# Optimization experiments

Hardware: AMD Instinct MI355X
Metric: run time of the kernel (lower is better)

Reference implementation:

```python
import jax, jax.numpy as jnp
import numpy as np

N, IN_C, OUT_C = 8192, 256, 256


def setup_inputs() -> dict:
    key = jax.random.key(0)
    k1, k2, k3 = jax.random.split(key, 3)
    x = jax.random.normal(k1, (N, IN_C), dtype=jnp.float32)
    adj = jax.random.uniform(k2, (N, N), dtype=jnp.float32)
    # learned parameter: torch.rand(in_channels, out_channels)
    w = jax.random.uniform(k3, (IN_C, OUT_C), dtype=jnp.float32)
    return {"x": x, "adj": adj, "w": w}


def reference(x, adj, w):
    # A = adj + I
    A = adj + jnp.eye(adj.shape[0], dtype=adj.dtype)
    # D_hat = sqrt(inv(diag(rowsum(A)))) == diag(deg^{-1/2}) since D is diagonal
    deg = jnp.sum(A, axis=1)                      # [N]
    d_isqrt = jax.lax.rsqrt(deg)                  # [N]
    # A_hat = D_hat @ A @ D_hat  ==  row/col scaling by d^{-1/2}
    A_hat = A * d_isqrt[:, None] * d_isqrt[None, :]
    # ELU((A_hat @ x) @ w)
    h = jnp.matmul(A_hat, x)                      # [N, in_c]
    return jax.nn.elu(jnp.matmul(h, w))           # [N, out_c]
```

## Files before the change

### kernel.cpp

```cpp
#include <hip/hip_runtime.h>
#include <stdint.h>

#define N_NODES 8192
#define CH 256
#define MT 32
#define BK 64
#define KB_COUNT 128
#define NSTAGE 4
#define ZROWS 16
#define ZBLOCKS (N_NODES / ZROWS)
#define DEGBLOCKS (N_NODES / 4)

typedef __bf16 bf16x8 __attribute__((ext_vector_type(8)));
typedef float f32x4 __attribute__((ext_vector_type(4)));
typedef unsigned short u16x4 __attribute__((ext_vector_type(4)));

__device__ __forceinline__ void async_copy16(const void* g, void* l) {
  __builtin_amdgcn_global_load_lds(
      (const __attribute__((address_space(1))) void*)(uintptr_t)g,
      (__attribute__((address_space(3))) void*)(uint32_t)(uintptr_t)l,
      16, 0, 0);
}

__device__ __forceinline__ unsigned short f32_to_bf16_rne(float f) {
  unsigned u = __float_as_uint(f);
  u += 0x7FFFu + ((u >> 16) & 1u);
  return (unsigned short)(u >> 16);
}

__device__ __forceinline__ u16x4 f32x4_to_bf16_rne(f32x4 v) {
  u16x4 r;
  r.x = f32_to_bf16_rne(v.x);
  r.y = f32_to_bf16_rne(v.y);
  r.z = f32_to_bf16_rne(v.z);
  r.w = f32_to_bf16_rne(v.w);
  return r;
}

__global__ void __launch_bounds__(256) k_pass1(const float* __restrict__ x,
                                               const float* __restrict__ w,
                                               const float* __restrict__ adj,
                                               float* __restrict__ z,
                                               float* __restrict__ dsq,
                                               unsigned short* __restrict__ adjb) {
  __shared__ float xs[ZROWS][CH];
  if (blockIdx.x < ZBLOCKS) {
    const int r0 = blockIdx.x * ZROWS;
    const int t = threadIdx.x;
#pragma unroll
    for (int r = 0; r < ZROWS; ++r) xs[r][t] = x[(size_t)(r0 + r) * CH + t];
    __syncthreads();
    float acc[ZROWS];
#pragma unroll
    for (int r = 0; r < ZROWS; ++r) acc[r] = 0.f;
    for (int k = 0; k < CH; k += 8) {
      float wv[8];
#pragma unroll
      for (int u = 0; u < 8; ++u) wv[u] = w[(size_t)(k + u) * CH + t];
#pragma unroll
      for (int r = 0; r < ZROWS; ++r) {
#pragma unroll
        for (int u = 0; u < 8; ++u) acc[r] += xs[r][k + u] * wv[u];
      }
    }
#pragma unroll
    for (int r = 0; r < ZROWS; ++r) z[(size_t)(r0 + r) * CH + t] = acc[r];
  } else {
    const int wave = threadIdx.x >> 6, lane = threadIdx.x & 63;
    const int row = (blockIdx.x - ZBLOCKS) * 4 + wave;
    const f32x4* ar = (const f32x4*)(adj + (size_t)row * N_NODES);
    u16x4* br = (u16x4*)(adjb + (size_t)row * N_NODES);
    float s0 = 0.f, s1 = 0.f, s2 = 0.f, s3 = 0.f;
#pragma unroll
    for (int i = 0; i < 8; ++i) {
      f32x4 a = ar[lane + 64 * (4 * i + 0)];
      f32x4 b = ar[lane + 64 * (4 * i + 1)];
      f32x4 c = ar[lane + 64 * (4 * i + 2)];
      f32x4 d = ar[lane + 64 * (4 * i + 3)];
      br[lane + 64 * (4 * i + 0)] = f32x4_to_bf16_rne(a);
      br[lane + 64 * (4 * i + 1)] = f32x4_to_bf16_rne(b);
      br[lane + 64 * (4 * i + 2)] = f32x4_to_bf16_rne(c);
      br[lane + 64 * (4 * i + 3)] = f32x4_to_bf16_rne(d);
      s0 += (a.x + a.y) + (a.z + a.w);
      s1 += (b.x + b.y) + (b.z + b.w);
      s2 += (c.x + c.y) + (c.z + c.w);
      s3 += (d.x + d.y) + (d.z + d.w);
    }
    float s = (s0 + s1) + (s2 + s3);
#pragma unroll
    for (int off = 32; off > 0; off >>= 1) s += __shfl_down(s, off, 64);
    if (lane == 0) dsq[row] = rsqrtf(s + 1.0f);
  }
}

__global__ void __launch_bounds__(256) k_y(const float* __restrict__ z,
                                           const float* __restrict__ dsq,
                                           unsigned short* __restrict__ yt) {
  const int r0 = blockIdx.x * 16;
  const int t = threadIdx.x;
  unsigned short vals[16];
#pragma unroll
  for (int r = 0; r < 16; ++r)
    vals[r] = f32_to_bf16_rne(dsq[r0 + r] * z[(size_t)(r0 + r) * CH + t]);
  *(u16x4*)&yt[(size_t)t * N_NODES + r0 + 0] = *(u16x4*)&vals[0];
  *(u16x4*)&yt[(size_t)t * N_NODES + r0 + 4] = *(u16x4*)&vals[4];
  *(u16x4*)&yt[(size_t)t * N_NODES + r0 + 8] = *(u16x4*)&vals[8];
  *(u16x4*)&yt[(size_t)t * N_NODES + r0 + 12] = *(u16x4*)&vals[12];
}

__global__ void __launch_bounds__(512, 1) k_gemm1(const unsigned short* __restrict__ adjb,
                                                  const unsigned short* __restrict__ yt,
                                                  const float* __restrict__ z,
                                                  const float* __restrict__ dsq,
                                                  float* __restrict__ out) {
  __shared__ __align__(16) unsigned short As[NSTAGE][MT * BK];
  __shared__ __align__(16) unsigned short Bs[NSTAGE][CH * BK];

  const int tid = threadIdx.x;
  const int wave = tid >> 6;
  const int lane = tid & 63;
  const int m0 = blockIdx.x * MT;
  const int lr = lane & 15;
  const int lq = lane >> 4;

  const bool hasA = wave < 4;
  const unsigned short* ag;
  int aoffu;
  {
    int i = hasA ? wave : 0;
    int p = 64 * i + lane;
    int r = p >> 3;
    int c8 = (lane & 7) ^ (r & 7);
    ag = adjb + (size_t)(m0 + r) * N_NODES + c8 * 8;
    aoffu = 1024 * i;
  }
  const unsigned short* bg[4];
  int boffu[4];
#pragma unroll
  for (int q = 0; q < 4; ++q) {
    int i = wave * 4 + q;
    int p = 64 * i + lane;
    int n = p >> 3;
    int c8 = (lane & 7) ^ (n & 7);
    bg[q] = yt + (size_t)n * N_NODES + c8 * 8;
    boffu[q] = 1024 * i;
  }

  f32x4 acc[2][2];
#pragma unroll
  for (int i = 0; i < 2; ++i)
#pragma unroll
    for (int j = 0; j < 2; ++j) acc[i][j] = (f32x4){0.f, 0.f, 0.f, 0.f};

  auto issue = [&](int b, int k0) {
    char* aL = (char*)&As[b][0];
    char* bL = (char*)&Bs[b][0];
    if (hasA) async_copy16(ag + k0, aL + aoffu);
#pragma unroll
    for (int q = 0; q < 4; ++q) async_copy16(bg[q] + k0, bL + boffu[q]);
  };

  auto compute = [&](int b) {
    const char* aB = (const char*)&As[b][0];
    const char* bB = (const char*)&Bs[b][0];
#pragma unroll
    for (int k32 = 0; k32 < 2; ++k32) {
      bf16x8 afr[2];
#pragma unroll
      for (int mt = 0; mt < 2; ++mt) {
        int row = mt * 16 + lr;
        int c8 = k32 * 4 + lq;
        int p = row * 8 + (c8 ^ (row & 7));
        afr[mt] = *(const bf16x8*)(aB + p * 16);
      }
      __builtin_amdgcn_s_setprio(1);
#pragma unroll
      for (int nt = 0; nt < 2; ++nt) {
        int n = wave * 32 + nt * 16 + lr;
        int c8 = k32 * 4 + lq;
        int p = n * 8 + (c8 ^ (n & 7));
        bf16x8 bfr = *(const bf16x8*)(bB + p * 16);
        acc[0][nt] = __builtin_amdgcn_mfma_f32_16x16x32_bf16(afr[0], bfr, acc[0][nt], 0, 0, 0);
        acc[1][nt] = __builtin_amdgcn_mfma_f32_16x16x32_bf16(afr[1], bfr, acc[1][nt], 0, 0, 0);
      }
      __builtin_amdgcn_s_setprio(0);
    }
  };

  issue(0, 0);
  issue(1, BK);
  issue(2, 2 * BK);

  for (int kb = 0; kb < KB_COUNT - 2; ++kb) {
    if (hasA) asm volatile("s_waitcnt vmcnt(10)" ::: "memory");
    else      asm volatile("s_waitcnt vmcnt(8)"  ::: "memory");
    __builtin_amdgcn_s_barrier();
    __builtin_amdgcn_sched_barrier(0);
    if (kb + 3 < KB_COUNT) issue((kb + 3) & (NSTAGE - 1), (kb + 3) * BK);
    compute(kb & (NSTAGE - 1));
    __builtin_amdgcn_sched_barrier(0);
  }
  if (hasA) asm volatile("s_waitcnt vmcnt(5)" ::: "memory");
  else      asm volatile("s_waitcnt vmcnt(4)" ::: "memory");
  __builtin_amdgcn_s_barrier();
  __builtin_amdgcn_sched_barrier(0);
  compute((KB_COUNT - 2) & (NSTAGE - 1));
  __builtin_amdgcn_sched_barrier(0);
  asm volatile("s_waitcnt vmcnt(0)" ::: "memory");
  __builtin_amdgcn_s_barrier();
  __builtin_amdgcn_sched_barrier(0);
  compute((KB_COUNT - 1) & (NSTAGE - 1));

#pragma unroll
  for (int mt = 0; mt < 2; ++mt) {
#pragma unroll
    for (int r = 0; r < 4; ++r) {
      int row = m0 + mt * 16 + lq * 4 + r;
      float di = dsq[row];
#pragma unroll
      for (int nt = 0; nt < 2; ++nt) {
        int col = wave * 32 + nt * 16 + lr;
        float v = acc[mt][nt][r];
        v = di * (v + di * z[(size_t)row * CH + col]);
        v = v > 0.f ? v : expm1f(v);
        out[(size_t)row * CH + col] = v;
      }
    }
  }
}

extern "C" void kernel_launch(void* const* d_in, const int* in_sizes, int n_in,
                              void* d_out, int out_size, void* d_ws, size_t ws_size,
                              hipStream_t stream) {
  const float* x = (const float*)d_in[0];
  const float* adj = (const float*)d_in[1];
  const float* w = (const float*)d_in[2];
  float* out = (float*)d_out;

  float* dsq = (float*)d_ws;
  unsigned short* yt = (unsigned short*)((char*)d_ws + 32768);
  float* z = (float*)((char*)d_ws + 4227072);
  unsigned short* adjb = (unsigned short*)((char*)d_ws + 12615680);

  k_pass1<<<ZBLOCKS + DEGBLOCKS, 256, 0, stream>>>(x, w, adj, z, dsq, adjb);
  k_y<<<N_NODES / 16, 256, 0, stream>>>(z, dsq, yt);
  k_gemm1<<<N_NODES / MT, 512, 0, stream>>>(adjb, yt, z, dsq, out);
}
```

Before: 480.6 us.

## Use 128-row tiles with 4-way split-K and a separate finalize kernel

```diff
diff --git a/kernel.cpp b/kernel.cpp
--- a/kernel.cpp
+++ b/kernel.cpp
@@ -3,10 +3,12 @@
 
 #define N_NODES 8192
 #define CH 256
-#define MT 32
+#define BM 128
 #define BK 64
-#define KB_COUNT 128
-#define NSTAGE 4
+#define KSPLIT 4
+#define KLEN (N_NODES / KSPLIT)
+#define TILES (KLEN / BK)
+#define NSTAGE 3
 #define ZROWS 16
 #define ZBLOCKS (N_NODES / ZROWS)
 #define DEGBLOCKS (N_NODES / 4)
@@ -110,54 +112,57 @@
 
 __global__ void __launch_bounds__(512, 1) k_gemm1(const unsigned short* __restrict__ adjb,
                                                   const unsigned short* __restrict__ yt,
-                                                  const float* __restrict__ z,
-                                                  const float* __restrict__ dsq,
-                                                  float* __restrict__ out) {
-  __shared__ __align__(16) unsigned short As[NSTAGE][MT * BK];
+                                                  float* __restrict__ part) {
+  __shared__ __align__(16) unsigned short As[NSTAGE][BM * BK];
   __shared__ __align__(16) unsigned short Bs[NSTAGE][CH * BK];
 
   const int tid = threadIdx.x;
   const int wave = tid >> 6;
   const int lane = tid & 63;
-  const int m0 = blockIdx.x * MT;
+  const int s = blockIdx.x & 3;
+  const int m0 = (blockIdx.x >> 2) * BM;
+  const int k_base = s * KLEN;
   const int lr = lane & 15;
   const int lq = lane >> 4;
-
-  const bool hasA = wave < 4;
-  const unsigned short* ag;
-  int aoffu;
-  {
-    int i = hasA ? wave : 0;
+  const int wr = wave >> 2;
+  const int wc = wave & 3;
+
+  const unsigned short* ag[2];
+  int aoff[2];
+#pragma unroll
+  for (int q = 0; q < 2; ++q) {
+    int i = wave * 2 + q;
     int p = 64 * i + lane;
     int r = p >> 3;
     int c8 = (lane & 7) ^ (r & 7);
-    ag = adjb + (size_t)(m0 + r) * N_NODES + c8 * 8;
-    aoffu = 1024 * i;
+    ag[q] = adjb + (size_t)(m0 + r) * N_NODES + k_base + c8 * 8;
+    aoff[q] = 1024 * i;
   }
   const unsigned short* bg[4];
-  int boffu[4];
+  int boff[4];
 #pragma unroll
   for (int q = 0; q < 4; ++q) {
     int i = wave * 4 + q;
     int p = 64 * i + lane;
     int n = p >> 3;
     int c8 = (lane & 7) ^ (n & 7);
-    bg[q] = yt + (size_t)n * N_NODES + c8 * 8;
-    boffu[q] = 1024 * i;
-  }
-
-  f32x4 acc[2][2];
-#pragma unroll
-  for (int i = 0; i < 2; ++i)
-#pragma unroll
-    for (int j = 0; j < 2; ++j) acc[i][j] = (f32x4){0.f, 0.f, 0.f, 0.f};
+    bg[q] = yt + (size_t)n * N_NODES + k_base + c8 * 8;
+    boff[q] = 1024 * i;
+  }
+
+  f32x4 acc[4][4];
+#pragma unroll
+  for (int i = 0; i < 4; ++i)
+#pragma unroll
+    for (int j = 0; j < 4; ++j) acc[i][j] = (f32x4){0.f, 0.f, 0.f, 0.f};
 
   auto issue = [&](int b, int k0) {
     char* aL = (char*)&As[b][0];
     char* bL = (char*)&Bs[b][0];
-    if (hasA) async_copy16(ag + k0, aL + aoffu);
-#pragma unroll
-    for (int q = 0; q < 4; ++q) async_copy16(bg[q] + k0, bL + boffu[q]);
+#pragma unroll
+    for (int q = 0; q < 2; ++q) async_copy16(ag[q] + k0, aL + aoff[q]);
+#pragma unroll
+    for (int q = 0; q < 4; ++q) async_copy16(bg[q] + k0, bL + boff[q]);
   };
 
   auto compute = [&](int b) {
@@ -165,23 +170,23 @@
     const char* bB = (const char*)&Bs[b][0];
 #pragma unroll
     for (int k32 = 0; k32 < 2; ++k32) {
-      bf16x8 afr[2];
-#pragma unroll
-      for (int mt = 0; mt < 2; ++mt) {
-        int row = mt * 16 + lr;
-        int c8 = k32 * 4 + lq;
+      const int c8 = k32 * 4 + lq;
+      bf16x8 afr[4];
+#pragma unroll
+      for (int mt = 0; mt < 4; ++mt) {
+        int row = wr * 64 + mt * 16 + lr;
         int p = row * 8 + (c8 ^ (row & 7));
         afr[mt] = *(const bf16x8*)(aB + p * 16);
       }
       __builtin_amdgcn_s_setprio(1);
 #pragma unroll
-      for (int nt = 0; nt < 2; ++nt) {
-        int n = wave * 32 + nt * 16 + lr;
-        int c8 = k32 * 4 + lq;
+      for (int nt = 0; nt < 4; ++nt) {
+        int n = wc * 64 + nt * 16 + lr;
         int p = n * 8 + (c8 ^ (n & 7));
         bf16x8 bfr = *(const bf16x8*)(bB + p * 16);
-        acc[0][nt] = __builtin_amdgcn_mfma_f32_16x16x32_bf16(afr[0], bfr, acc[0][nt], 0, 0, 0);
-        acc[1][nt] = __builtin_amdgcn_mfma_f32_16x16x32_bf16(afr[1], bfr, acc[1][nt], 0, 0, 0);
+#pragma unroll
+        for (int mt = 0; mt < 4; ++mt)
+          acc[mt][nt] = __builtin_amdgcn_mfma_f32_16x16x32_bf16(afr[mt], bfr, acc[mt][nt], 0, 0, 0);
       }
       __builtin_amdgcn_s_setprio(0);
     }
@@ -189,43 +194,57 @@
 
   issue(0, 0);
   issue(1, BK);
-  issue(2, 2 * BK);
-
-  for (int kb = 0; kb < KB_COUNT - 2; ++kb) {
-    if (hasA) asm volatile("s_waitcnt vmcnt(10)" ::: "memory");
-    else      asm volatile("s_waitcnt vmcnt(8)"  ::: "memory");
+
+  int bc = 0;
+  for (int kb = 0; kb < TILES - 1; ++kb) {
+    asm volatile("s_waitcnt vmcnt(6)" ::: "memory");
     __builtin_amdgcn_s_barrier();
     __builtin_amdgcn_sched_barrier(0);
-    if (kb + 3 < KB_COUNT) issue((kb + 3) & (NSTAGE - 1), (kb + 3) * BK);
-    compute(kb & (NSTAGE - 1));
+    if (kb + 2 < TILES) {
+      int bi = bc + 2;
+      if (bi >= NSTAGE) bi -= NSTAGE;
+      issue(bi, (kb + 2) * BK);
+    }
+    compute(bc);
     __builtin_amdgcn_sched_barrier(0);
-  }
-  if (hasA) asm volatile("s_waitcnt vmcnt(5)" ::: "memory");
-  else      asm volatile("s_waitcnt vmcnt(4)" ::: "memory");
-  __builtin_amdgcn_s_barrier();
-  __builtin_amdgcn_sched_barrier(0);
-  compute((KB_COUNT - 2) & (NSTAGE - 1));
-  __builtin_amdgcn_sched_barrier(0);
+    bc = (bc + 1 == NSTAGE) ? 0 : bc + 1;
+  }
   asm volatile("s_waitcnt vmcnt(0)" ::: "memory");
   __builtin_amdgcn_s_barrier();
   __builtin_amdgcn_sched_barrier(0);
-  compute((KB_COUNT - 1) & (NSTAGE - 1));
-
-#pragma unroll
-  for (int mt = 0; mt < 2; ++mt) {
+  compute(bc);
+
+  float* Ps = part + (size_t)s * N_NODES * CH;
+#pragma unroll
+  for (int mt = 0; mt < 4; ++mt) {
 #pragma unroll
     for (int r = 0; r < 4; ++r) {
-      int row = m0 + mt * 16 + lq * 4 + r;
-      float di = dsq[row];
-#pragma unroll
-      for (int nt = 0; nt < 2; ++nt) {
-        int col = wave * 32 + nt * 16 + lr;
-        float v = acc[mt][nt][r];
-        v = di * (v + di * z[(size_t)row * CH + col]);
-        v = v > 0.f ? v : expm1f(v);
-        out[(size_t)row * CH + col] = v;
-      }
-    }
+      int row = m0 + wr * 64 + mt * 16 + lq * 4 + r;
+#pragma unroll
+      for (int nt = 0; nt < 4; ++nt) {
+        int col = wc * 64 + nt * 16 + lr;
+        Ps[(size_t)row * CH + col] = acc[mt][nt][r];
+      }
+    }
+  }
+}
+
+__global__ void __launch_bounds__(256) k_fin(const float* __restrict__ part,
+                                             const float* __restrict__ z,
+                                             const float* __restrict__ dsq,
+                                             float* __restrict__ out) {
+  const int r0 = blockIdx.x * 16;
+  const int t = threadIdx.x;
+  const size_t SP = (size_t)N_NODES * CH;
+#pragma unroll
+  for (int r = 0; r < 16; ++r) {
+    const int row = r0 + r;
+    const size_t idx = (size_t)row * CH + t;
+    float sum = (part[idx] + part[idx + SP]) + (part[idx + 2 * SP] + part[idx + 3 * SP]);
+    float di = dsq[row];
+    float v = di * (sum + di * z[idx]);
+    v = v > 0.f ? v : expm1f(v);
+    out[idx] = v;
   }
 }
 
@@ -241,8 +260,10 @@
   unsigned short* yt = (unsigned short*)((char*)d_ws + 32768);
   float* z = (float*)((char*)d_ws + 4227072);
   unsigned short* adjb = (unsigned short*)((char*)d_ws + 12615680);
+  float* part = (float*)((char*)d_ws + 146833408);
 
   k_pass1<<<ZBLOCKS + DEGBLOCKS, 256, 0, stream>>>(x, w, adj, z, dsq, adjb);
   k_y<<<N_NODES / 16, 256, 0, stream>>>(z, dsq, yt);
-  k_gemm1<<<N_NODES / MT, 512, 0, stream>>>(adjb, yt, z, dsq, out);
-}
+  k_gemm1<<<N_NODES / BM * KSPLIT, 512, 0, stream>>>(adjb, yt, part);
+  k_fin<<<N_NODES / 16, 256, 0, stream>>>(part, z, dsq, out);
+}
```

Result: faster. 444.6 us (-7.5%).
